# Performance work log

Measured on AMD Instinct MI355X. Metric: run time of the kernel, lower is better.

## Reference

```python
import jax, jax.numpy as jnp
import numpy as np

D = 512
VOCAB = 8192
UTT_LEN = 16
BATCH = 32
NTYPES = 8
MPT = 32
NLAYERS = 2


def setup_inputs() -> dict:
    key = jax.random.key(0)
    ks = jax.random.split(key, 16)
    d, dff, v1 = D, 4 * D, VOCAB + 1
    s = 0.02
    nrm = lambda k, shape: jax.random.normal(k, shape, dtype=jnp.float32) * s
    zeros = lambda shape: jnp.zeros(shape, jnp.float32)
    ones = lambda shape: jnp.ones(shape, jnp.float32)
    return {
        'meanings': jax.random.randint(ks[0], (BATCH, NTYPES), 0, MPT),
        'emb_table': nrm(ks[1], (NTYPES * MPT, d)),
        'v2e_w': nrm(ks[2], (v1, d)),
        'e2v_w': nrm(ks[3], (v1, d)),
        'e2v_b': zeros((v1,)),
        'sa_qkv_w': nrm(ks[4], (NLAYERS, 3 * d, d)),
        'sa_qkv_b': zeros((NLAYERS, 3 * d)),
        'sa_out_w': nrm(ks[5], (NLAYERS, d, d)),
        'sa_out_b': zeros((NLAYERS, d)),
        'ca_qkv_w': nrm(ks[6], (NLAYERS, 3 * d, d)),
        'ca_qkv_b': zeros((NLAYERS, 3 * d)),
        'ca_out_w': nrm(ks[7], (NLAYERS, d, d)),
        'ca_out_b': zeros((NLAYERS, d)),
        'ffn_w1': nrm(ks[8], (NLAYERS, dff, d)),
        'ffn_b1': zeros((NLAYERS, dff)),
        'ffn_w2': nrm(ks[9], (NLAYERS, d, dff)),
        'ffn_b2': zeros((NLAYERS, d)),
        'ln1_g': ones((NLAYERS, d)), 'ln1_b': zeros((NLAYERS, d)),
        'ln2_g': ones((NLAYERS, d)), 'ln2_b': zeros((NLAYERS, d)),
        'ln3_g': ones((NLAYERS, d)), 'ln3_b': zeros((NLAYERS, d)),
    }


def _ln(x, g, b, eps=1e-5):
    m = x.mean(-1, keepdims=True)
    v = ((x - m) ** 2).mean(-1, keepdims=True)
    return (x - m) / jnp.sqrt(v + eps) * g + b


def _attn(q_in, kv_in, qkv_w, qkv_b, out_w, out_b, mask):
    # single-head attention, torch MultiheadAttention layout (seq, batch, d)
    d = q_in.shape[-1]
    q = q_in @ qkv_w[:d].T + qkv_b[:d]
    k = kv_in @ qkv_w[d:2 * d].T + qkv_b[d:2 * d]
    v = kv_in @ qkv_w[2 * d:].T + qkv_b[2 * d:]
    scores = jnp.einsum('qbd,kbd->bqk', q, k) / jnp.sqrt(jnp.float32(d))
    if mask is not None:
        scores = scores + mask
    a = jax.nn.softmax(scores, axis=-1)
    o = jnp.einsum('bqk,kbd->qbd', a, v)
    return o @ out_w.T + out_b


def _sinusoidal_pe(L, d):
    pos = np.arange(L)[:, None].astype(np.float32)
    div = np.exp(np.arange(0, d, 2).astype(np.float32) * (-np.log(10000.0) / d))
    pe = np.zeros((L, d), np.float32)
    pe[:, 0::2] = np.sin(pos * div)
    pe[:, 1::2] = np.cos(pos * div)
    return jnp.asarray(pe)[:, None, :]  # [L,1,d]


def reference(meanings, emb_table, v2e_w, e2v_w, e2v_b,
              sa_qkv_w, sa_qkv_b, sa_out_w, sa_out_b,
              ca_qkv_w, ca_qkv_b, ca_out_w, ca_out_b,
              ffn_w1, ffn_b1, ffn_w2, ffn_b2,
              ln1_g, ln1_b, ln2_g, ln2_b, ln3_g, ln3_b):
    B, T = meanings.shape
    v1, d = v2e_w.shape
    start_token = v1 - 1
    mpt = emb_table.shape[0] // T
    offs = jnp.arange(T, dtype=meanings.dtype) * mpt
    src = emb_table[meanings + offs].sum(axis=1)[None]  # [1,B,d] cross-attn memory
    L = UTT_LEN
    pe = _sinusoidal_pe(L, d)
    causal = jnp.where(jnp.tril(jnp.ones((L, L), bool)), 0.0, -jnp.inf).astype(jnp.float32)
    nlayers = sa_qkv_w.shape[0]

    def step(buf, i):
        # full-length decode with causal mask == original growing-prefix decode at position i
        x = v2e_w[buf[:L]] + pe  # [L,B,d]
        for l in range(nlayers):
            sa = _attn(x, x, sa_qkv_w[l], sa_qkv_b[l], sa_out_w[l], sa_out_b[l], causal)
            x = _ln(x + sa, ln1_g[l], ln1_b[l])
            ca = _attn(x, src, ca_qkv_w[l], ca_qkv_b[l], ca_out_w[l], ca_out_b[l], None)
            x = _ln(x + ca, ln2_g[l], ln2_b[l])
            ff = jax.nn.relu(x @ ffn_w1[l].T + ffn_b1[l]) @ ffn_w2[l].T + ffn_b2[l]
            x = _ln(x + ff, ln3_g[l], ln3_b[l])
        h = jnp.take(x, i, axis=0)         # [B,d] last generated position
        logits = h @ e2v_w.T + e2v_b        # [B,V+1]
        tok = jnp.argmax(logits, axis=-1).astype(buf.dtype)
        buf = buf.at[i + 1].set(tok)
        return buf, (tok, logits)

    buf0 = jnp.zeros((L + 1, B), jnp.int32).at[0].set(start_token)
    _, (toks, logits) = jax.lax.scan(step, buf0, jnp.arange(L))
    return toks, logits  # utterances [utt_len,B], per-step logits [utt_len,B,V+1]
```

## Files before the change

### kernel.cpp

```cpp
#include <hip/hip_runtime.h>
#include <cmath>

namespace {

constexpr int Dm  = 512;
constexpr int Bn  = 32;
constexpr int Lq  = 16;
constexpr int V1  = 8193;
constexpr int DFF = 2048;
constexpr int NL  = 2;
constexpr int NT  = 256;

__device__ __forceinline__ float wred(float v) {
#pragma unroll
  for (int off = 32; off; off >>= 1) v += __shfl_down(v, off, 64);
  return v;
}

__device__ __forceinline__ float dot4(const float4 w, const float4 x, float a) {
  a = fmaf(w.x, x.x, a); a = fmaf(w.y, x.y, a);
  a = fmaf(w.z, x.z, a); a = fmaf(w.w, x.w, a);
  return a;
}

__device__ __forceinline__ float pe_val(int pos, int t) {
  const int j2 = (t >> 1) << 1;
  const float div = expf((float)j2 * (-9.210340371976184f / 512.0f));
  const float ang = (float)pos * div;
  return (t & 1) ? cosf(ang) : sinf(ang);
}

template <int KS, int Kc, int SP, bool RELU, int ROWS>
__global__ __launch_bounds__(NT) void fg_part(
    const float* __restrict__ xsrc, int xstride, int pstride,
    const float* __restrict__ W, int K, const float* __restrict__ bias,
    float* __restrict__ part, int N) {
  constexpr int QR = Kc / 4;
  constexpr int RH = ROWS / 2;
  __shared__ float smem[32 * Kc];
  const int bid = (int)blockIdx.x, tid = (int)threadIdx.x;
  const int kc = bid % KS, k0 = kc * Kc;
  for (int idx = tid; idx < 8 * Kc; idx += NT) {
    const int b = idx / QR, q = idx - b * QR;
    const float* s0 = xsrc + (size_t)b * xstride + k0 + (q << 2);
    float4 v = *(const float4*)(s0);
#pragma unroll
    for (int s = 1; s < SP; ++s) {
      const float4 u = *(const float4*)(s0 + (size_t)s * pstride);
      v.x += u.x; v.y += u.y; v.z += u.z; v.w += u.w;
    }
    if (RELU) {
      v.x = fmaxf(v.x, 0.f); v.y = fmaxf(v.y, 0.f);
      v.z = fmaxf(v.z, 0.f); v.w = fmaxf(v.w, 0.f);
    }
    *(float4*)(smem + b * Kc + ((q ^ (b & 7)) << 2)) = v;
  }
  __syncthreads();
  const int lane = tid & 63, wave = tid >> 6;
  const int bl = lane & 31, nh = lane >> 5, sw = bl & 7;
  const float* xb = smem + bl * Kc;
  const int rowjob = (bid / KS) * 4 + wave;
  const int n0 = rowjob * ROWS + nh * RH;
  const float* w = W + (size_t)n0 * K + k0;
  float a[RH];
#pragma unroll
  for (int r = 0; r < RH; ++r) a[r] = 0.f;
#pragma unroll 4
  for (int qq = 0; qq < QR; ++qq) {
    const float4 xv = *(const float4*)(xb + ((qq ^ sw) << 2));
    const float* wq = w + (qq << 2);
#pragma unroll
    for (int r = 0; r < RH; ++r)
      a[r] = dot4(*(const float4*)(wq + (size_t)r * K), xv, a[r]);
  }
  if (kc == 0) {
#pragma unroll
    for (int r = 0; r < RH; ++r) a[r] += bias[n0 + r];
  }
  float* yb = part + (size_t)kc * 32 * N + (size_t)bl * N + n0;
#pragma unroll
  for (int r = 0; r < RH; ++r) yb[r] = a[r];
}

__global__ __launch_bounds__(NT) void fg_qkv_part(const float* __restrict__ x,
    const float* __restrict__ W, const float* __restrict__ bias,
    float* __restrict__ qkvp) {
  constexpr int Kc = 64, QR = 16;
  __shared__ float smem[32 * Kc];
  const int bid = (int)blockIdx.x, tid = (int)threadIdx.x;
  const int kc = bid & 7, k0 = kc << 6;
  for (int idx = tid; idx < 8 * Kc; idx += NT) {
    const int b = idx / QR, q = idx - b * QR;
    const float4 v = *(const float4*)(x + (b << 9) + k0 + (q << 2));
    *(float4*)(smem + b * Kc + ((q ^ (b & 7)) << 2)) = v;
  }
  __syncthreads();
  const int lane = tid & 63, wave = tid >> 6;
  const int bl = lane & 31, nh = lane >> 5, sw = bl & 7;
  const float* xb = smem + bl * Kc;
  const int rowjob = (bid >> 3) * 4 + wave;
  const int n0 = (rowjob << 2) + (nh << 1);
  const float* w = W + (size_t)n0 * Dm + k0;
  float a0 = 0.f, a1 = 0.f;
#pragma unroll 4
  for (int qq = 0; qq < QR; ++qq) {
    const float4 xv = *(const float4*)(xb + ((qq ^ sw) << 2));
    const float* wq = w + (qq << 2);
    a0 = dot4(*(const float4*)(wq), xv, a0);
    a1 = dot4(*(const float4*)(wq + Dm), xv, a1);
  }
  if (kc == 0) { a0 += bias[n0]; a1 += bias[n0 + 1]; }
  const int seg = n0 >> 9;
  float* yb = qkvp + (size_t)seg * 131072 + (size_t)kc * 16384 + (bl << 9) + (n0 & 511);
  yb[0] = a0; yb[1] = a1;
}

__device__ __forceinline__ void block_ln(float* s, const float* __restrict__ g,
                                         const float* __restrict__ bb, float* red) {
  const int tid = (int)threadIdx.x;
  float ls = 0.f, lq = 0.f;
  for (int t = tid; t < Dm; t += NT) { const float v = s[t]; ls += v; lq += v * v; }
  ls = wred(ls); lq = wred(lq);
  const int wave = tid >> 6, lane = tid & 63;
  if (lane == 0) { red[wave] = ls; red[4 + wave] = lq; }
  __syncthreads();
  const float sum = red[0] + red[1] + red[2] + red[3];
  const float sq  = red[4] + red[5] + red[6] + red[7];
  const float mean = sum * (1.f / Dm);
  const float var  = sq * (1.f / Dm) - mean * mean;
  const float inv  = 1.f / sqrtf(var + 1e-5f);
  __syncthreads();
  for (int t = tid; t < Dm; t += NT) s[t] = (s[t] - mean) * inv * g[t] + bb[t];
}

__global__ __launch_bounds__(NT) void attn_core(const float* __restrict__ qkvp,
    float* __restrict__ kcl, float* __restrict__ vcl,
    float* __restrict__ aout, int pos) {
  __shared__ float sQ[Dm], sK[Dm], sV[Dm], sS[Lq];
  const int b = (int)blockIdx.x, tid = (int)threadIdx.x;
  const int lane = tid & 63, wave = tid >> 6;
  const float* qp = qkvp;
  const float* kp = qkvp + 131072;
  const float* vp = qkvp + 262144;
  for (int t = tid; t < Dm; t += NT) {
    const int o = (b << 9) + t;
    float qv = 0.f, kv = 0.f, vv = 0.f;
#pragma unroll
    for (int s = 0; s < 8; ++s) {
      qv += qp[o + s * 16384]; kv += kp[o + s * 16384]; vv += vp[o + s * 16384];
    }
    sQ[t] = qv; sK[t] = kv; sV[t] = vv;
    const int co = ((pos * Bn + b) << 9) + t;
    kcl[co] = kv; vcl[co] = vv;
  }
  __syncthreads();
  for (int j = wave; j <= pos; j += 4) {
    float acc;
    if (j == pos) {
      acc = dot4(*(const float4*)(sK + (lane << 2)),
                 *(const float4*)(sQ + (lane << 2)), 0.f);
      acc = dot4(*(const float4*)(sK + 256 + (lane << 2)),
                 *(const float4*)(sQ + 256 + (lane << 2)), acc);
    } else {
      const float* kr = kcl + ((size_t)(j * Bn + b) << 9);
      acc = dot4(*(const float4*)(kr + (lane << 2)),
                 *(const float4*)(sQ + (lane << 2)), 0.f);
      acc = dot4(*(const float4*)(kr + 256 + (lane << 2)),
                 *(const float4*)(sQ + 256 + (lane << 2)), acc);
    }
    acc = wred(acc);
    if (lane == 0) sS[j] = acc * 0.044194173824159216f;
  }
  __syncthreads();
  if (tid == 0) {
    float m = -1e30f;
    for (int j = 0; j <= pos; ++j) m = fmaxf(m, sS[j]);
    float s = 0.f;
    for (int j = 0; j <= pos; ++j) { const float e = expf(sS[j] - m); sS[j] = e; s += e; }
    const float inv = 1.f / s;
    for (int j = 0; j <= pos; ++j) sS[j] *= inv;
  }
  __syncthreads();
  for (int t = tid; t < Dm; t += NT) {
    float acc = sS[pos] * sV[t];
    for (int j = 0; j < pos; ++j) acc += sS[j] * vcl[((size_t)(j * Bn + b) << 9) + t];
    aout[(b << 9) + t] = acc;
  }
}

__global__ __launch_bounds__(NT) void ln12(const float* __restrict__ sop,
    const float* __restrict__ caCp,
    const float* __restrict__ g1, const float* __restrict__ b1,
    const float* __restrict__ g2, const float* __restrict__ b2,
    float* __restrict__ x) {
  __shared__ float sR[Dm], red[8];
  const int b = (int)blockIdx.x, tid = (int)threadIdx.x;
  for (int t = tid; t < Dm; t += NT) {
    const int o = (b << 9) + t;
    float v = x[o];
#pragma unroll
    for (int s = 0; s < 16; ++s) v += sop[o + s * 16384];
    sR[t] = v;
  }
  __syncthreads();
  block_ln(sR, g1, b1, red);
  __syncthreads();
  for (int t = tid; t < Dm; t += NT) {
    const int o = (b << 9) + t;
    float v = sR[t];
#pragma unroll
    for (int s = 0; s < 4; ++s) v += caCp[o + s * 16384];
    sR[t] = v;
  }
  __syncthreads();
  block_ln(sR, g2, b2, red);
  __syncthreads();
  for (int t = tid; t < Dm; t += NT) x[(b << 9) + t] = sR[t];
}

__global__ __launch_bounds__(NT) void ln3red(const float* __restrict__ f2p,
    const float* __restrict__ g3, const float* __restrict__ bb3,
    float* __restrict__ x) {
  __shared__ float sR[Dm], red[8];
  const int b = (int)blockIdx.x, tid = (int)threadIdx.x;
  for (int t = tid; t < Dm; t += NT) {
    const int o = (b << 9) + t;
    float v = x[o];
#pragma unroll
    for (int s = 0; s < 16; ++s) v += f2p[o + s * 16384];
    sR[t] = v;
  }
  __syncthreads();
  block_ln(sR, g3, bb3, red);
  __syncthreads();
  for (int t = tid; t < Dm; t += NT) x[(b << 9) + t] = sR[t];
}

__global__ __launch_bounds__(512) void src_kernel(const int* __restrict__ meanings,
                                                  const float* __restrict__ emb,
                                                  float* __restrict__ src) {
  const int b = (int)blockIdx.x, t = (int)threadIdx.x;
  float s = 0.f;
#pragma unroll
  for (int ty = 0; ty < 8; ++ty) {
    const int idx = meanings[b * 8 + ty] + ty * 32;
    s += emb[(size_t)idx * Dm + t];
  }
  src[b * Dm + t] = s;
}

__global__ __launch_bounds__(512) void embed0(const float* __restrict__ v2e,
                                              float* __restrict__ x) {
  const int b = (int)blockIdx.x, t = (int)threadIdx.x;
  x[(b << 9) + t] = v2e[(size_t)(V1 - 1) * Dm + t] + pe_val(0, t);
}

__global__ __launch_bounds__(NT) void argmax_embed(float* __restrict__ x,
    const float* __restrict__ e2v_w, const float* __restrict__ e2v_b,
    const float* __restrict__ v2e, const float* __restrict__ lp,
    float* __restrict__ outLogits, float* __restrict__ outToks, int i) {
  __shared__ float red[8];
  __shared__ float sv[NT];
  __shared__ int   si[NT];
  const int b = (int)blockIdx.x, tid = (int)threadIdx.x;
  const int lane = tid & 63, wave = tid >> 6;
  float ls = 0.f;
  for (int t = tid; t < Dm; t += NT) ls += x[(b << 9) + t] * e2v_w[(size_t)8192 * Dm + t];
  ls = wred(ls);
  if (lane == 0) red[wave] = ls;
  __syncthreads();
  float* row = outLogits + ((size_t)i * Bn + b) * V1;
  if (tid == 0) {
    const float lg = red[0] + red[1] + red[2] + red[3] + e2v_b[8192];
    row[8192] = lg;
    red[4] = lg;
  }
  __syncthreads();
  const float lg = red[4];
  float best = -1e30f; int bi = 0;
  for (int v = tid; v < 8192; v += NT) {
    const float val = lp[(b << 13) + v] + lp[262144 + (b << 13) + v];
    row[v] = val;
    if (val > best) { best = val; bi = v; }
  }
  sv[tid] = best; si[tid] = bi;
  __syncthreads();
  for (int off = 128; off; off >>= 1) {
    if (tid < off) {
      const float v2 = sv[tid + off]; const int i2 = si[tid + off];
      if (v2 > sv[tid] || (v2 == sv[tid] && i2 < si[tid])) { sv[tid] = v2; si[tid] = i2; }
    }
    __syncthreads();
  }
  if (tid == 0) {
    int tok = si[0];
    if (lg > sv[0]) tok = 8192;
    outToks[i * Bn + b] = (float)tok;
    si[0] = tok;
  }
  __syncthreads();
  const int tok = si[0];
  if (i + 1 < Lq) {
    for (int t = tid; t < Dm; t += NT)
      x[(b << 9) + t] = v2e[(size_t)tok * Dm + t] + pe_val(i + 1, t);
  }
}

}

extern "C" void kernel_launch(void* const* d_in, const int* in_sizes, int n_in,
                              void* d_out, int out_size, void* d_ws, size_t ws_size,
                              hipStream_t stream) {
  (void)in_sizes; (void)n_in; (void)out_size; (void)ws_size;
  const int*   meanings  = (const int*)d_in[0];
  const float* emb_table = (const float*)d_in[1];
  const float* v2e_w     = (const float*)d_in[2];
  const float* e2v_w     = (const float*)d_in[3];
  const float* e2v_b     = (const float*)d_in[4];
  const float* sa_qkv_w  = (const float*)d_in[5];
  const float* sa_qkv_b  = (const float*)d_in[6];
  const float* sa_out_w  = (const float*)d_in[7];
  const float* sa_out_b  = (const float*)d_in[8];
  const float* ca_qkv_w  = (const float*)d_in[9];
  const float* ca_qkv_b  = (const float*)d_in[10];
  const float* ca_out_w  = (const float*)d_in[11];
  const float* ca_out_b  = (const float*)d_in[12];
  const float* ffn_w1    = (const float*)d_in[13];
  const float* ffn_b1    = (const float*)d_in[14];
  const float* ffn_w2    = (const float*)d_in[15];
  const float* ffn_b2    = (const float*)d_in[16];
  const float* ln1_g     = (const float*)d_in[17];
  const float* ln1_b     = (const float*)d_in[18];
  const float* ln2_g     = (const float*)d_in[19];
  const float* ln2_b     = (const float*)d_in[20];
  const float* ln3_g     = (const float*)d_in[21];
  const float* ln3_b     = (const float*)d_in[22];

  float* out = (float*)d_out;
  float* outLogits = out + Lq * Bn;

  float* f = (float*)d_ws;
  float* src  = f;  f += 16384;
  float* x    = f;  f += 16384;
  float* aout = f;  f += 16384;
  float* caCp = f;  f += 131072;
  float* A    = f;  f += 524288;
  float* f2p  = f;  f += 262144;
  float* kcache = f; f += 524288;
  float* vcache = f;

  src_kernel<<<Bn, 512, 0, stream>>>(meanings, emb_table, src);

  for (int l = 0; l < NL; ++l) {
    fg_part<4, 128, 1, false, 8><<<64, NT, 0, stream>>>(src, Dm, 0,
        ca_qkv_w + ((size_t)l * 3 + 2) * Dm * Dm, Dm,
        ca_qkv_b + l * 3 * Dm + 2 * Dm, A, Dm);
    fg_part<4, 128, 4, false, 8><<<64, NT, 0, stream>>>(A, Dm, 16384,
        ca_out_w + (size_t)l * Dm * Dm, Dm,
        ca_out_b + l * Dm, caCp + (size_t)l * 65536, Dm);
  }

  embed0<<<Bn, 512, 0, stream>>>(v2e_w, x);

  for (int i = 0; i < Lq; ++i) {
    for (int l = 0; l < NL; ++l) {
      float* kcl = kcache + (size_t)l * Lq * Bn * Dm;
      float* vcl = vcache + (size_t)l * Lq * Bn * Dm;
      fg_qkv_part<<<768, NT, 0, stream>>>(x,
          sa_qkv_w + (size_t)l * 3 * Dm * Dm, sa_qkv_b + l * 3 * Dm, A);
      attn_core<<<Bn, NT, 0, stream>>>(A, kcl, vcl, aout, i);
      fg_part<16, 32, 1, false, 4><<<512, NT, 0, stream>>>(aout, Dm, 0,
          sa_out_w + (size_t)l * Dm * Dm, Dm, sa_out_b + l * Dm, A, Dm);
      ln12<<<Bn, NT, 0, stream>>>(A, caCp + (size_t)l * 65536,
          ln1_g + l * Dm, ln1_b + l * Dm, ln2_g + l * Dm, ln2_b + l * Dm, x);
      fg_part<8, 64, 1, false, 4><<<1024, NT, 0, stream>>>(x, Dm, 0,
          ffn_w1 + (size_t)l * DFF * Dm, Dm, ffn_b1 + l * DFF, A, DFF);
      fg_part<16, 128, 8, true, 4><<<512, NT, 0, stream>>>(A, DFF, 65536,
          ffn_w2 + (size_t)l * Dm * DFF, DFF, ffn_b2 + l * Dm, f2p, Dm);
      ln3red<<<Bn, NT, 0, stream>>>(f2p,
          ln3_g + l * Dm, ln3_b + l * Dm, x);
    }
    fg_part<2, 256, 1, false, 4><<<1024, NT, 0, stream>>>(x, Dm, 0,
        e2v_w, Dm, e2v_b, A, 8192);
    argmax_embed<<<Bn, NT, 0, stream>>>(x, e2v_w, e2v_b, v2e_w, A,
        outLogits, out, i);
  }
}
```

Baseline: 2.261 ms.

## Fuse split-K GEMMs with their reductions using last-arriving-block tickets

```diff
diff --git a/kernel.cpp b/kernel.cpp
--- a/kernel.cpp
+++ b/kernel.cpp
@@ -11,6 +11,24 @@
 constexpr int NL  = 2;
 constexpr int NT  = 256;
 
+__device__ __forceinline__ float g_ld(const float* p) {
+  return __hip_atomic_load(p, __ATOMIC_RELAXED, __HIP_MEMORY_SCOPE_AGENT);
+}
+__device__ __forceinline__ float2 g_ld2(const float* p) {
+  unsigned long long u = __hip_atomic_load((const unsigned long long*)p,
+      __ATOMIC_RELAXED, __HIP_MEMORY_SCOPE_AGENT);
+  float2 r;
+  r.x = __uint_as_float((unsigned)u);
+  r.y = __uint_as_float((unsigned)(u >> 32));
+  return r;
+}
+__device__ __forceinline__ void g_st2(float* p, float a, float b) {
+  unsigned long long u = (unsigned long long)__float_as_uint(a) |
+                         ((unsigned long long)__float_as_uint(b) << 32);
+  __hip_atomic_store((unsigned long long*)p, u, __ATOMIC_RELAXED,
+                     __HIP_MEMORY_SCOPE_AGENT);
+}
+
 __device__ __forceinline__ float wred(float v) {
 #pragma unroll
   for (int off = 32; off; off >>= 1) v += __shfl_down(v, off, 64);
@@ -28,6 +46,56 @@
   const float div = expf((float)j2 * (-9.210340371976184f / 512.0f));
   const float ang = (float)pos * div;
   return (t & 1) ? cosf(ang) : sinf(ang);
+}
+
+__device__ __forceinline__ void wait_ctr(const unsigned* c, unsigned n) {
+  if (threadIdx.x == 0) {
+    while (__hip_atomic_load(c, __ATOMIC_RELAXED, __HIP_MEMORY_SCOPE_AGENT) < n)
+      __builtin_amdgcn_s_sleep(2);
+    asm volatile("" ::: "memory");
+  }
+  __syncthreads();
+}
+
+__device__ __forceinline__ void block_ln(float* s, const float* __restrict__ g,
+                                         const float* __restrict__ bb, float* red) {
+  const int tid = (int)threadIdx.x;
+  float ls = 0.f, lq = 0.f;
+  for (int t = tid; t < Dm; t += NT) { const float v = s[t]; ls += v; lq += v * v; }
+  ls = wred(ls); lq = wred(lq);
+  const int wave = tid >> 6, lane = tid & 63;
+  if (lane == 0) { red[wave] = ls; red[4 + wave] = lq; }
+  __syncthreads();
+  const float sum = red[0] + red[1] + red[2] + red[3];
+  const float sq  = red[4] + red[5] + red[6] + red[7];
+  const float mean = sum * (1.f / Dm);
+  const float var  = sq * (1.f / Dm) - mean * mean;
+  const float inv  = 1.f / sqrtf(var + 1e-5f);
+  __syncthreads();
+  for (int t = tid; t < Dm; t += NT) s[t] = (s[t] - mean) * inv * g[t] + bb[t];
+}
+
+__global__ __launch_bounds__(512) void init_bar(unsigned* bar) {
+  const int i = (int)blockIdx.x * 512 + (int)threadIdx.x;
+  __hip_atomic_store(bar + i, 0u, __ATOMIC_RELAXED, __HIP_MEMORY_SCOPE_AGENT);
+}
+
+__global__ __launch_bounds__(512) void src_kernel(const int* __restrict__ meanings,
+    const float* __restrict__ emb, float* __restrict__ src) {
+  const int b = (int)blockIdx.x, t = (int)threadIdx.x;
+  float s = 0.f;
+#pragma unroll
+  for (int ty = 0; ty < 8; ++ty) {
+    const int idx = meanings[b * 8 + ty] + ty * 32;
+    s += emb[(size_t)idx * Dm + t];
+  }
+  src[b * Dm + t] = s;
+}
+
+__global__ __launch_bounds__(512) void embed0(const float* __restrict__ v2e,
+                                              float* __restrict__ x) {
+  const int b = (int)blockIdx.x, t = (int)threadIdx.x;
+  x[(b << 9) + t] = v2e[(size_t)(V1 - 1) * Dm + t] + pe_val(0, t);
 }
 
 template <int KS, int Kc, int SP, bool RELU, int ROWS>
@@ -82,63 +150,50 @@
   for (int r = 0; r < RH; ++r) yb[r] = a[r];
 }
 
-__global__ __launch_bounds__(NT) void fg_qkv_part(const float* __restrict__ x,
+__global__ __launch_bounds__(NT) void k_qkv_attn(const float* __restrict__ x,
     const float* __restrict__ W, const float* __restrict__ bias,
-    float* __restrict__ qkvp) {
-  constexpr int Kc = 64, QR = 16;
-  __shared__ float smem[32 * Kc];
+    float* __restrict__ qkvp, float* __restrict__ kcl, float* __restrict__ vcl,
+    float* __restrict__ aout, unsigned* ctr, int pos) {
+  __shared__ float smem[2048];
+  __shared__ int tkt_s;
   const int bid = (int)blockIdx.x, tid = (int)threadIdx.x;
-  const int kc = bid & 7, k0 = kc << 6;
-  for (int idx = tid; idx < 8 * Kc; idx += NT) {
-    const int b = idx / QR, q = idx - b * QR;
-    const float4 v = *(const float4*)(x + (b << 9) + k0 + (q << 2));
-    *(float4*)(smem + b * Kc + ((q ^ (b & 7)) << 2)) = v;
-  }
-  __syncthreads();
   const int lane = tid & 63, wave = tid >> 6;
-  const int bl = lane & 31, nh = lane >> 5, sw = bl & 7;
-  const float* xb = smem + bl * Kc;
-  const int rowjob = (bid >> 3) * 4 + wave;
-  const int n0 = (rowjob << 2) + (nh << 1);
-  const float* w = W + (size_t)n0 * Dm + k0;
-  float a0 = 0.f, a1 = 0.f;
+  {
+    constexpr int Kc = 64, QR = 16;
+    const int kc = bid & 7, k0 = kc << 6;
+    for (int idx = tid; idx < 512; idx += NT) {
+      const int b = idx / QR, q = idx - b * QR;
+      const float4 v = *(const float4*)(x + (b << 9) + k0 + (q << 2));
+      *(float4*)(smem + b * Kc + ((q ^ (b & 7)) << 2)) = v;
+    }
+    __syncthreads();
+    const int bl = lane & 31, nh = lane >> 5, sw = bl & 7;
+    const float* xb = smem + bl * Kc;
+    const int rowjob = (bid >> 3) * 4 + wave;
+    const int n0 = (rowjob << 2) + (nh << 1);
+    const float* w = W + (size_t)n0 * Dm + k0;
+    float a0 = 0.f, a1 = 0.f;
 #pragma unroll 4
-  for (int qq = 0; qq < QR; ++qq) {
-    const float4 xv = *(const float4*)(xb + ((qq ^ sw) << 2));
-    const float* wq = w + (qq << 2);
-    a0 = dot4(*(const float4*)(wq), xv, a0);
-    a1 = dot4(*(const float4*)(wq + Dm), xv, a1);
-  }
-  if (kc == 0) { a0 += bias[n0]; a1 += bias[n0 + 1]; }
-  const int seg = n0 >> 9;
-  float* yb = qkvp + (size_t)seg * 131072 + (size_t)kc * 16384 + (bl << 9) + (n0 & 511);
-  yb[0] = a0; yb[1] = a1;
-}
-
-__device__ __forceinline__ void block_ln(float* s, const float* __restrict__ g,
-                                         const float* __restrict__ bb, float* red) {
-  const int tid = (int)threadIdx.x;
-  float ls = 0.f, lq = 0.f;
-  for (int t = tid; t < Dm; t += NT) { const float v = s[t]; ls += v; lq += v * v; }
-  ls = wred(ls); lq = wred(lq);
-  const int wave = tid >> 6, lane = tid & 63;
-  if (lane == 0) { red[wave] = ls; red[4 + wave] = lq; }
-  __syncthreads();
-  const float sum = red[0] + red[1] + red[2] + red[3];
-  const float sq  = red[4] + red[5] + red[6] + red[7];
-  const float mean = sum * (1.f / Dm);
-  const float var  = sq * (1.f / Dm) - mean * mean;
-  const float inv  = 1.f / sqrtf(var + 1e-5f);
-  __syncthreads();
-  for (int t = tid; t < Dm; t += NT) s[t] = (s[t] - mean) * inv * g[t] + bb[t];
-}
-
-__global__ __launch_bounds__(NT) void attn_core(const float* __restrict__ qkvp,
-    float* __restrict__ kcl, float* __restrict__ vcl,
-    float* __restrict__ aout, int pos) {
-  __shared__ float sQ[Dm], sK[Dm], sV[Dm], sS[Lq];
-  const int b = (int)blockIdx.x, tid = (int)threadIdx.x;
-  const int lane = tid & 63, wave = tid >> 6;
+    for (int qq = 0; qq < QR; ++qq) {
+      const float4 xv = *(const float4*)(xb + ((qq ^ sw) << 2));
+      const float* wq = w + (qq << 2);
+      a0 = dot4(*(const float4*)(wq), xv, a0);
+      a1 = dot4(*(const float4*)(wq + Dm), xv, a1);
+    }
+    if (kc == 0) { a0 += bias[n0]; a1 += bias[n0 + 1]; }
+    const int seg = n0 >> 9;
+    float* yb = qkvp + (size_t)seg * 131072 + (size_t)kc * 16384 + (bl << 9) + (n0 & 511);
+    g_st2(yb, a0, a1);
+  }
+  __syncthreads();
+  if (tid == 0)
+    tkt_s = (int)__hip_atomic_fetch_add(ctr, 1u, __ATOMIC_RELEASE, __HIP_MEMORY_SCOPE_AGENT);
+  __syncthreads();
+  if (tkt_s < 736) return;
+  const int b = tkt_s - 736;
+  wait_ctr(ctr, 768);
+  float* sQ = smem; float* sK = smem + 512; float* sV = smem + 1024;
+  float* sS = smem + 1536;
   const float* qp = qkvp;
   const float* kp = qkvp + 131072;
   const float* vp = qkvp + 262144;
@@ -147,7 +202,9 @@
     float qv = 0.f, kv = 0.f, vv = 0.f;
 #pragma unroll
     for (int s = 0; s < 8; ++s) {
-      qv += qp[o + s * 16384]; kv += kp[o + s * 16384]; vv += vp[o + s * 16384];
+      qv += g_ld(qp + o + s * 16384);
+      kv += g_ld(kp + o + s * 16384);
+      vv += g_ld(vp + o + s * 16384);
     }
     sQ[t] = qv; sK[t] = kv; sV[t] = vv;
     const int co = ((pos * Bn + b) << 9) + t;
@@ -188,22 +245,61 @@
   }
 }
 
-__global__ __launch_bounds__(NT) void ln12(const float* __restrict__ sop,
+__global__ __launch_bounds__(NT) void k_saout_ln12(const float* __restrict__ aout,
+    const float* __restrict__ W, const float* __restrict__ bias,
+    float* __restrict__ sop, float* __restrict__ x,
     const float* __restrict__ caCp,
     const float* __restrict__ g1, const float* __restrict__ b1,
     const float* __restrict__ g2, const float* __restrict__ b2,
-    float* __restrict__ x) {
-  __shared__ float sR[Dm], red[8];
-  const int b = (int)blockIdx.x, tid = (int)threadIdx.x;
+    unsigned* ctr) {
+  __shared__ float smem[1024];
+  __shared__ float red_s[8];
+  __shared__ int tkt_s;
+  const int bid = (int)blockIdx.x, tid = (int)threadIdx.x;
+  const int lane = tid & 63, wave = tid >> 6;
+  {
+    constexpr int Kc = 32, QR = 8;
+    const int kc = bid & 15, k0 = kc << 5;
+    for (int idx = tid; idx < 256; idx += NT) {
+      const int b = idx / QR, q = idx - b * QR;
+      const float4 v = *(const float4*)(aout + (b << 9) + k0 + (q << 2));
+      *(float4*)(smem + b * Kc + ((q ^ (b & 7)) << 2)) = v;
+    }
+    __syncthreads();
+    const int bl = lane & 31, nh = lane >> 5, sw = bl & 7;
+    const float* xb = smem + bl * Kc;
+    const int rowjob = (bid >> 4) * 4 + wave;
+    const int n0 = (rowjob << 2) + (nh << 1);
+    const float* w = W + (size_t)n0 * Dm + k0;
+    float a0 = 0.f, a1 = 0.f;
+#pragma unroll
+    for (int qq = 0; qq < QR; ++qq) {
+      const float4 xv = *(const float4*)(xb + ((qq ^ sw) << 2));
+      const float* wq = w + (qq << 2);
+      a0 = dot4(*(const float4*)(wq), xv, a0);
+      a1 = dot4(*(const float4*)(wq + Dm), xv, a1);
+    }
+    if (kc == 0) { a0 += bias[n0]; a1 += bias[n0 + 1]; }
+    float* yb = sop + (size_t)kc * 16384 + (bl << 9) + n0;
+    g_st2(yb, a0, a1);
+  }
+  __syncthreads();
+  if (tid == 0)
+    tkt_s = (int)__hip_atomic_fetch_add(ctr, 1u, __ATOMIC_RELEASE, __HIP_MEMORY_SCOPE_AGENT);
+  __syncthreads();
+  if (tkt_s < 480) return;
+  const int b = tkt_s - 480;
+  wait_ctr(ctr, 512);
+  float* sR = smem;
   for (int t = tid; t < Dm; t += NT) {
     const int o = (b << 9) + t;
     float v = x[o];
 #pragma unroll
-    for (int s = 0; s < 16; ++s) v += sop[o + s * 16384];
+    for (int s = 0; s < 16; ++s) v += g_ld(sop + o + s * 16384);
     sR[t] = v;
   }
   __syncthreads();
-  block_ln(sR, g1, b1, red);
+  block_ln(sR, g1, b1, red_s);
   __syncthreads();
   for (int t = tid; t < Dm; t += NT) {
     const int o = (b << 9) + t;
@@ -213,59 +309,124 @@
     sR[t] = v;
   }
   __syncthreads();
-  block_ln(sR, g2, b2, red);
+  block_ln(sR, g2, b2, red_s);
   __syncthreads();
   for (int t = tid; t < Dm; t += NT) x[(b << 9) + t] = sR[t];
 }
 
-__global__ __launch_bounds__(NT) void ln3red(const float* __restrict__ f2p,
-    const float* __restrict__ g3, const float* __restrict__ bb3,
-    float* __restrict__ x) {
-  __shared__ float sR[Dm], red[8];
-  const int b = (int)blockIdx.x, tid = (int)threadIdx.x;
+__global__ __launch_bounds__(NT) void k_ffn2_ln3(const float* __restrict__ h1p,
+    const float* __restrict__ W, const float* __restrict__ bias,
+    float* __restrict__ f2p, float* __restrict__ x,
+    const float* __restrict__ g3, const float* __restrict__ b3,
+    unsigned* ctr) {
+  __shared__ float smem[4096];
+  __shared__ float red_s[8];
+  __shared__ int tkt_s;
+  const int bid = (int)blockIdx.x, tid = (int)threadIdx.x;
+  const int lane = tid & 63, wave = tid >> 6;
+  {
+    constexpr int Kc = 128, QR = 32;
+    const int kc = bid & 15, k0 = kc << 7;
+    for (int idx = tid; idx < 1024; idx += NT) {
+      const int b = idx / QR, q = idx - b * QR;
+      const float* s0 = h1p + (size_t)b * DFF + k0 + (q << 2);
+      float4 v = *(const float4*)(s0);
+#pragma unroll
+      for (int s = 1; s < 8; ++s) {
+        const float4 u = *(const float4*)(s0 + (size_t)s * 65536);
+        v.x += u.x; v.y += u.y; v.z += u.z; v.w += u.w;
+      }
+      v.x = fmaxf(v.x, 0.f); v.y = fmaxf(v.y, 0.f);
+      v.z = fmaxf(v.z, 0.f); v.w = fmaxf(v.w, 0.f);
+      *(float4*)(smem + b * Kc + ((q ^ (b & 7)) << 2)) = v;
+    }
+    __syncthreads();
+    const int bl = lane & 31, nh = lane >> 5, sw = bl & 7;
+    const float* xb = smem + bl * Kc;
+    const int rowjob = (bid >> 4) * 4 + wave;
+    const int n0 = (rowjob << 2) + (nh << 1);
+    const float* w = W + (size_t)n0 * DFF + k0;
+    float a0 = 0.f, a1 = 0.f;
+#pragma unroll 4
+    for (int qq = 0; qq < QR; ++qq) {
+      const float4 xv = *(const float4*)(xb + ((qq ^ sw) << 2));
+      const float* wq = w + (qq << 2);
+      a0 = dot4(*(const float4*)(wq), xv, a0);
+      a1 = dot4(*(const float4*)(wq + DFF), xv, a1);
+    }
+    if (kc == 0) { a0 += bias[n0]; a1 += bias[n0 + 1]; }
+    float* yb = f2p + (size_t)kc * 16384 + (bl << 9) + n0;
+    g_st2(yb, a0, a1);
+  }
+  __syncthreads();
+  if (tid == 0)
+    tkt_s = (int)__hip_atomic_fetch_add(ctr, 1u, __ATOMIC_RELEASE, __HIP_MEMORY_SCOPE_AGENT);
+  __syncthreads();
+  if (tkt_s < 480) return;
+  const int b = tkt_s - 480;
+  wait_ctr(ctr, 512);
+  float* sR = smem;
   for (int t = tid; t < Dm; t += NT) {
     const int o = (b << 9) + t;
     float v = x[o];
 #pragma unroll
-    for (int s = 0; s < 16; ++s) v += f2p[o + s * 16384];
+    for (int s = 0; s < 16; ++s) v += g_ld(f2p + o + s * 16384);
     sR[t] = v;
   }
   __syncthreads();
-  block_ln(sR, g3, bb3, red);
+  block_ln(sR, g3, b3, red_s);
   __syncthreads();
   for (int t = tid; t < Dm; t += NT) x[(b << 9) + t] = sR[t];
 }
 
-__global__ __launch_bounds__(512) void src_kernel(const int* __restrict__ meanings,
-                                                  const float* __restrict__ emb,
-                                                  float* __restrict__ src) {
-  const int b = (int)blockIdx.x, t = (int)threadIdx.x;
-  float s = 0.f;
-#pragma unroll
-  for (int ty = 0; ty < 8; ++ty) {
-    const int idx = meanings[b * 8 + ty] + ty * 32;
-    s += emb[(size_t)idx * Dm + t];
-  }
-  src[b * Dm + t] = s;
-}
-
-__global__ __launch_bounds__(512) void embed0(const float* __restrict__ v2e,
-                                              float* __restrict__ x) {
-  const int b = (int)blockIdx.x, t = (int)threadIdx.x;
-  x[(b << 9) + t] = v2e[(size_t)(V1 - 1) * Dm + t] + pe_val(0, t);
-}
-
-__global__ __launch_bounds__(NT) void argmax_embed(float* __restrict__ x,
+__global__ __launch_bounds__(NT) void k_logits_argmax(float* __restrict__ x,
     const float* __restrict__ e2v_w, const float* __restrict__ e2v_b,
-    const float* __restrict__ v2e, const float* __restrict__ lp,
-    float* __restrict__ outLogits, float* __restrict__ outToks, int i) {
-  __shared__ float red[8];
-  __shared__ float sv[NT];
-  __shared__ int   si[NT];
-  const int b = (int)blockIdx.x, tid = (int)threadIdx.x;
+    const float* __restrict__ v2e, float* __restrict__ lp,
+    float* __restrict__ outLogits, float* __restrict__ outToks,
+    unsigned* ctr, int i) {
+  __shared__ float smem[8192];
+  __shared__ int tkt_s;
+  const int bid = (int)blockIdx.x, tid = (int)threadIdx.x;
   const int lane = tid & 63, wave = tid >> 6;
+  {
+    constexpr int Kc = 256, QR = 64;
+    const int kc = bid & 1, k0 = kc << 8;
+    for (int idx = tid; idx < 2048; idx += NT) {
+      const int b = idx / QR, q = idx - b * QR;
+      const float4 v = *(const float4*)(x + (b << 9) + k0 + (q << 2));
+      *(float4*)(smem + b * Kc + ((q ^ (b & 7)) << 2)) = v;
+    }
+    __syncthreads();
+    const int bl = lane & 31, nh = lane >> 5, sw = bl & 7;
+    const float* xb = smem + bl * Kc;
+    const int rowjob = (bid >> 1) * 4 + wave;
+    const int n0 = (rowjob << 2) + (nh << 1);
+    const float* w = e2v_w + (size_t)n0 * Dm + k0;
+    float a0 = 0.f, a1 = 0.f;
+#pragma unroll 4
+    for (int qq = 0; qq < QR; ++qq) {
+      const float4 xv = *(const float4*)(xb + ((qq ^ sw) << 2));
+      const float* wq = w + (qq << 2);
+      a0 = dot4(*(const float4*)(wq), xv, a0);
+      a1 = dot4(*(const float4*)(wq + Dm), xv, a1);
+    }
+    if (kc == 0) { a0 += e2v_b[n0]; a1 += e2v_b[n0 + 1]; }
+    float* yb = lp + (size_t)kc * 262144 + (size_t)bl * 8192 + n0;
+    g_st2(yb, a0, a1);
+  }
+  __syncthreads();
+  if (tid == 0)
+    tkt_s = (int)__hip_atomic_fetch_add(ctr, 1u, __ATOMIC_RELEASE, __HIP_MEMORY_SCOPE_AGENT);
+  __syncthreads();
+  if (tkt_s < 992) return;
+  const int b = tkt_s - 992;
+  wait_ctr(ctr, 1024);
+  float* red = smem;
+  float* sv  = smem + 8;
+  int*   si  = (int*)(smem + 8 + NT);
   float ls = 0.f;
-  for (int t = tid; t < Dm; t += NT) ls += x[(b << 9) + t] * e2v_w[(size_t)8192 * Dm + t];
+  for (int t = tid; t < Dm; t += NT)
+    ls += x[(b << 9) + t] * e2v_w[(size_t)8192 * Dm + t];
   ls = wred(ls);
   if (lane == 0) red[wave] = ls;
   __syncthreads();
@@ -278,10 +439,13 @@
   __syncthreads();
   const float lg = red[4];
   float best = -1e30f; int bi = 0;
-  for (int v = tid; v < 8192; v += NT) {
-    const float val = lp[(b << 13) + v] + lp[262144 + (b << 13) + v];
-    row[v] = val;
-    if (val > best) { best = val; bi = v; }
+  for (int v0 = tid * 2; v0 < 8192; v0 += NT * 2) {
+    const float2 a = g_ld2(lp + (b << 13) + v0);
+    const float2 c = g_ld2(lp + 262144 + (b << 13) + v0);
+    const float va = a.x + c.x, vb = a.y + c.y;
+    row[v0] = va; row[v0 + 1] = vb;
+    if (va > best) { best = va; bi = v0; }
+    if (vb > best) { best = vb; bi = v0 + 1; }
   }
   sv[tid] = best; si[tid] = bi;
   __syncthreads();
@@ -339,7 +503,9 @@
   float* out = (float*)d_out;
   float* outLogits = out + Lq * Bn;
 
-  float* f = (float*)d_ws;
+  char* ws = (char*)d_ws;
+  unsigned* bar = (unsigned*)ws;
+  float* f = (float*)(ws + 32768);
   float* src  = f;  f += 16384;
   float* x    = f;  f += 16384;
   float* aout = f;  f += 16384;
@@ -349,6 +515,9 @@
   float* kcache = f; f += 524288;
   float* vcache = f;
 
+  int cidx = 0;
+
+  init_bar<<<16, 512, 0, stream>>>(bar);
   src_kernel<<<Bn, 512, 0, stream>>>(meanings, emb_table, src);
 
   for (int l = 0; l < NL; ++l) {
@@ -366,23 +535,21 @@
     for (int l = 0; l < NL; ++l) {
       float* kcl = kcache + (size_t)l * Lq * Bn * Dm;
       float* vcl = vcache + (size_t)l * Lq * Bn * Dm;
-      fg_qkv_part<<<768, NT, 0, stream>>>(x,
-          sa_qkv_w + (size_t)l * 3 * Dm * Dm, sa_qkv_b + l * 3 * Dm, A);
-      attn_core<<<Bn, NT, 0, stream>>>(A, kcl, vcl, aout, i);
-      fg_part<16, 32, 1, false, 4><<<512, NT, 0, stream>>>(aout, Dm, 0,
-          sa_out_w + (size_t)l * Dm * Dm, Dm, sa_out_b + l * Dm, A, Dm);
-      ln12<<<Bn, NT, 0, stream>>>(A, caCp + (size_t)l * 65536,
-          ln1_g + l * Dm, ln1_b + l * Dm, ln2_g + l * Dm, ln2_b + l * Dm, x);
+      k_qkv_attn<<<768, NT, 0, stream>>>(x,
+          sa_qkv_w + (size_t)l * 3 * Dm * Dm, sa_qkv_b + l * 3 * Dm,
+          A, kcl, vcl, aout, bar + (cidx++) * 32, i);
+      k_saout_ln12<<<512, NT, 0, stream>>>(aout,
+          sa_out_w + (size_t)l * Dm * Dm, sa_out_b + l * Dm,
+          A, x, caCp + (size_t)l * 65536,
+          ln1_g + l * Dm, ln1_b + l * Dm, ln2_g + l * Dm, ln2_b + l * Dm,
+          bar + (cidx++) * 32);
       fg_part<8, 64, 1, false, 4><<<1024, NT, 0, stream>>>(x, Dm, 0,
           ffn_w1 + (size_t)l * DFF * Dm, Dm, ffn_b1 + l * DFF, A, DFF);
-      fg_part<16, 128, 8, true, 4><<<512, NT, 0, stream>>>(A, DFF, 65536,
-          ffn_w2 + (size_t)l * Dm * DFF, DFF, ffn_b2 + l * Dm, f2p, Dm);
-      ln3red<<<Bn, NT, 0, stream>>>(f2p,
-          ln3_g + l * Dm, ln3_b + l * Dm, x);
-    }
-    fg_part<2, 256, 1, false, 4><<<1024, NT, 0, stream>>>(x, Dm, 0,
-        e2v_w, Dm, e2v_b, A, 8192);
-    argmax_embed<<<Bn, NT, 0, stream>>>(x, e2v_w, e2v_b, v2e_w, A,
-        outLogits, out, i);
-  }
-}
+      k_ffn2_ln3<<<512, NT, 0, stream>>>(A,
+          ffn_w2 + (size_t)l * Dm * DFF, ffn_b2 + l * Dm,
+          f2p, x, ln3_g + l * Dm, ln3_b + l * Dm, bar + (cidx++) * 32);
+    }
+    k_logits_argmax<<<1024, NT, 0, stream>>>(x, e2v_w, e2v_b, v2e_w, A,
+        outLogits, out, bar + (cidx++) * 32, i);
+  }
+}
```

New measurement: 2.998 ms. 32.6% more time.
